# Performance work log

Hardware: AMD Instinct MI355X
Metric: run time of the kernel (lower is better)

Reference implementation:

```python
import jax, jax.numpy as jnp
import numpy as np
import math

N_EMBD = 1024
N_HEAD_DIM = 64
B, S = 8, 2048

def setup_inputs() -> dict:
    key = jax.random.key(0)
    ks = jax.random.split(key, 8)
    x = jax.random.normal(ks[0], (B, S, N_EMBD), dtype=jnp.float32)
    padding_mask = jax.random.randint(ks[1], (B, S), 0, 2).astype(jnp.bool_)
    scale = 1.0 / math.sqrt(N_EMBD)
    Wq = jax.random.normal(ks[2], (N_HEAD_DIM, N_EMBD), dtype=jnp.float32) * scale
    bq = jnp.zeros((N_HEAD_DIM,), dtype=jnp.float32)
    Wk = jax.random.normal(ks[3], (N_HEAD_DIM, N_EMBD), dtype=jnp.float32) * scale
    bk = jnp.zeros((N_HEAD_DIM,), dtype=jnp.float32)
    Wv = jax.random.normal(ks[4], (N_HEAD_DIM, N_EMBD), dtype=jnp.float32) * scale
    bv = jnp.zeros((N_HEAD_DIM,), dtype=jnp.float32)
    return {"x": x, "Wq": Wq, "bq": bq, "Wk": Wk, "bk": bk, "Wv": Wv, "bv": bv,
            "padding_mask": padding_mask}

def reference(x, Wq, bq, Wk, bk, Wv, bv, padding_mask):
    # q,k,v: [B,S,D] via Linear (x @ W^T + b)
    q = jnp.einsum('bse,de->bsd', x, Wq) + bq
    k = jnp.einsum('bse,de->bsd', x, Wk) + bk
    v = jnp.einsum('bse,de->bsd', x, Wv) + bv
    scale = 1.0 / math.sqrt(k.shape[-1])
    att = jnp.einsum('bqd,bkd->bqk', q, k) * scale  # [B,S,S]
    # padding_mask [B,S] -> [B,1,S]: True positions masked to -inf
    att = jnp.where(padding_mask[:, None, :], -jnp.inf, att)
    att = jax.nn.softmax(att, axis=-1)
    # attn_dropout omitted (eval mode / identity)
    return jnp.einsum('bqk,bkd->bqd', att, v)
```

## Files before the change

kernel.cpp:

```cpp
#include <hip/hip_runtime.h>
#include <hip/hip_bf16.h>

#define B_ 8
#define S_ 2048
#define E_ 1024
#define D_ 64
#define VT_STRIDE 2112

typedef short short8 __attribute__((ext_vector_type(8)));
typedef short short4v __attribute__((ext_vector_type(4)));
typedef float floatx4 __attribute__((ext_vector_type(4)));

static __device__ __forceinline__ short bf16_bits(float f) {
    __hip_bfloat16 h = __float2bfloat16(f);
    return *reinterpret_cast<short*>(&h);
}
static __device__ __forceinline__ float bits_to_f(short s) {
    __hip_bfloat16 h = *reinterpret_cast<__hip_bfloat16*>(&s);
    return __bfloat162float(h);
}
static __device__ __forceinline__ void split8(const float* __restrict__ p,
                                              short8& hi, short8& lo) {
    #pragma unroll
    for (int j = 0; j < 8; j++) {
        float f = p[j];
        short h = bf16_bits(f);
        hi[j] = h;
        lo[j] = bf16_bits(f - bits_to_f(h));
    }
}
static __device__ __forceinline__ void split8v(const float v[8],
                                               short8& hi, short8& lo) {
    #pragma unroll
    for (int j = 0; j < 8; j++) {
        float f = v[j];
        short h = bf16_bits(f);
        hi[j] = h;
        lo[j] = bf16_bits(f - bits_to_f(h));
    }
}
static __device__ __forceinline__ void dma16(const void* src, void* lds_dst) {
    __builtin_amdgcn_global_load_lds(
        (const __attribute__((address_space(1))) unsigned int*)src,
        (__attribute__((address_space(3))) unsigned int*)lds_dst, 16, 0, 0);
}

__global__ __launch_bounds__(256) void prep_kernel(
    const float* __restrict__ Wq, const float* __restrict__ Wk,
    const float* __restrict__ Wv, short8* __restrict__ Wpk8,
    const void* __restrict__ mask_raw, float* __restrict__ maskf)
{
    __shared__ unsigned int red[256];
    if (blockIdx.x < 96) {
        const int t = blockIdx.x * 256 + threadIdx.x;
        const int l16  = t & 15;
        const int quad = (t >> 4) & 3;
        const int nb   = (t >> 6) & 3;
        const int m    = (t >> 8) % 3;
        const int e0c  = (t >> 8) / 3;
        const float* W = (m == 0) ? Wq : ((m == 1) ? Wk : Wv);
        short8 hi, lo;
        split8(W + (size_t)(nb * 16 + l16) * E_ + e0c * 32 + quad * 8, hi, lo);
        const size_t pos = (size_t)((e0c * 3 + m) * 2) * 256 + nb * 64 + quad * 16 + l16;
        Wpk8[pos]       = hi;
        Wpk8[pos + 256] = lo;
    } else {
        const unsigned int* w = (const unsigned int*)mask_raw;
        unsigned int local = 0;
        for (int i = threadIdx.x; i < 4096; i += 256) local |= w[i];
        red[threadIdx.x] = local;
        __syncthreads();
        for (int s = 128; s > 0; s >>= 1) {
            if (threadIdx.x < s) red[threadIdx.x] |= red[threadIdx.x + s];
            __syncthreads();
        }
        const unsigned int ov = red[0];
        const bool is_u8 = (ov > 1u) && ((ov >> 24) <= 1u);
        const int i = (blockIdx.x - 96) * 256 + threadIdx.x;
        int v;
        if (ov == 0u)      v = 0;
        else if (is_u8)    v = (int)((const unsigned char*)mask_raw)[i];
        else               v = (((const unsigned int*)mask_raw)[i] != 0u);
        maskf[i] = v ? -1e30f : 0.0f;
    }
}

__global__ __launch_bounds__(512, 4) void qkv_kernel(
    const float* __restrict__ x, const short8* __restrict__ Wpk8,
    const float* __restrict__ bq, const float* __restrict__ bk,
    const float* __restrict__ bv,
    short* __restrict__ Qhi, short* __restrict__ Qlo,
    short* __restrict__ Khi, short* __restrict__ Vt)
{
    __shared__ alignas(16) float  xs[2][1024];
    __shared__ alignas(16) short8 wt[2][1536];
    const int tid  = threadIdx.x;
    const int wave = tid >> 6;
    const int nb   = wave & 3;
    const int rt   = wave >> 2;
    const int lane = tid & 63;
    const int l16  = lane & 15;
    const int quad = lane >> 4;
    const int row0 = blockIdx.x * 32;

    const float* xsrc = x + (size_t)(row0 + (tid >> 3)) * E_ +
                        (((tid & 7) ^ ((tid >> 3) & 7)) * 4);

    floatx4 acc[3];
    #pragma unroll
    for (int m = 0; m < 3; m++) acc[m] = (floatx4){0.f,0.f,0.f,0.f};

    if (tid < 256) dma16(xsrc, &xs[0][tid * 4]);
    #pragma unroll
    for (int i = 0; i < 3; i++)
        dma16(Wpk8 + (size_t)i * 512 + tid, &wt[0][i * 512 + tid]);

    int buf = 0;
    for (int e0c = 0; e0c < 32; ++e0c) {
        __syncthreads();
        if (e0c + 1 < 32) {
            if (tid < 256) dma16(xsrc + (e0c + 1) * 32, &xs[buf ^ 1][tid * 4]);
            #pragma unroll
            for (int i = 0; i < 3; i++)
                dma16(Wpk8 + (size_t)(e0c + 1) * 1536 + i * 512 + tid,
                      &wt[buf ^ 1][i * 512 + tid]);
        }

        const int rr = rt * 16 + l16;
        const int rx = rr & 7;
        const float* xr = &xs[buf][rr * 32];
        float4 a0 = *reinterpret_cast<const float4*>(xr + (((2 * quad)     ^ rx) * 4));
        float4 a1 = *reinterpret_cast<const float4*>(xr + (((2 * quad + 1) ^ rx) * 4));
        float av[8] = {a0.x, a0.y, a0.z, a0.w, a1.x, a1.y, a1.z, a1.w};
        short8 ah, al;
        split8v(av, ah, al);

        #pragma unroll
        for (int m = 0; m < 3; m++) {
            short8 wh = wt[buf][(m * 2 + 0) * 256 + nb * 64 + lane];
            short8 wl = wt[buf][(m * 2 + 1) * 256 + nb * 64 + lane];
            acc[m] = __builtin_amdgcn_mfma_f32_16x16x32_bf16(al, wh, acc[m], 0, 0, 0);
            acc[m] = __builtin_amdgcn_mfma_f32_16x16x32_bf16(ah, wl, acc[m], 0, 0, 0);
            acc[m] = __builtin_amdgcn_mfma_f32_16x16x32_bf16(ah, wh, acc[m], 0, 0, 0);
        }
        buf ^= 1;
    }

    const int d = nb * 16 + l16;
    const float bqv = bq[d];
    const float bkv = bk[d];
    const float bvv = bv[d];
    const int bch = row0 >> 11;
    const int rowbase = row0 + rt * 16 + quad * 4;
    short4v vpk;
    #pragma unroll
    for (int r = 0; r < 4; r++) {
        const size_t row = (size_t)(rowbase + r);
        const float q = (acc[0][r] + bqv) * 0.125f;
        const short qhv = bf16_bits(q);
        Qhi[row * 64 + d] = qhv;
        Qlo[row * 64 + d] = bf16_bits(q - bits_to_f(qhv));
        Khi[row * 64 + d] = bf16_bits(acc[1][r] + bkv);
        vpk[r] = bf16_bits(acc[2][r] + bvv);
    }
    *reinterpret_cast<short4v*>(Vt + ((size_t)(bch * 64 + d)) * VT_STRIDE +
                                (rowbase & 2047)) = vpk;
}

__global__ __launch_bounds__(256, 1) void attn_kernel(
    const short* __restrict__ Qhi, const short* __restrict__ Qlo,
    const short* __restrict__ Khi, const short* __restrict__ Vt,
    const float* __restrict__ maskf, float* __restrict__ out)
{
    __shared__ alignas(16) short8 kts[2][512];
    __shared__ alignas(16) short8 vts[2][512];
    __shared__ short PlT[4][16][72];

    const int tid  = threadIdx.x;
    const int wave = tid >> 6;
    const int lane = tid & 63;
    const int l16  = lane & 15;
    const int quad = lane >> 4;
    const int b    = blockIdx.x >> 5;
    const int qt   = blockIdx.x & 31;
    const size_t qbase  = (size_t)b * S_ + qt * 64 + wave * 16;
    const size_t kplane = (size_t)b * S_;
    const short* Vb = Vt + (size_t)b * 64 * VT_STRIDE;

    short8 qh[2], ql[2];
    #pragma unroll
    for (int dc = 0; dc < 2; dc++) {
        qh[dc] = *reinterpret_cast<const short8*>(Qhi + (qbase + l16) * 64 + dc * 32 + quad * 8);
        ql[dc] = *reinterpret_cast<const short8*>(Qlo + (qbase + l16) * 64 + dc * 32 + quad * 8);
    }

    float m = -1e30f, l = 0.f;
    floatx4 O[4];
    #pragma unroll
    for (int ob = 0; ob < 4; ob++) O[ob] = (floatx4){0.f,0.f,0.f,0.f};

    #pragma unroll
    for (int i = 0; i < 2; i++) {
        const int c = i * 256 + tid;
        const int r = c >> 3, cs = c & 7;
        dma16(Khi + (kplane + r) * 64 + ((cs ^ (r & 7)) * 8), &kts[0][c]);
        dma16(Vb + (size_t)r * VT_STRIDE + ((cs ^ (r & 7)) * 8), &vts[0][c]);
    }
    float4 mk4[4];
    #pragma unroll
    for (int kb = 0; kb < 4; kb++)
        mk4[kb] = *reinterpret_cast<const float4*>(maskf + kplane + kb * 16 + quad * 4);

    int buf = 0;
    for (int t = 0; t < 32; ++t) {
        __syncthreads();
        if (t + 1 < 32) {
            const int ktn = (t + 1) * 64;
            #pragma unroll
            for (int i = 0; i < 2; i++) {
                const int c = i * 256 + tid;
                const int r = c >> 3, cs = c & 7;
                dma16(Khi + (kplane + ktn + r) * 64 + ((cs ^ (r & 7)) * 8), &kts[buf ^ 1][c]);
                dma16(Vb + (size_t)r * VT_STRIDE + ktn + ((cs ^ (r & 7)) * 8), &vts[buf ^ 1][c]);
            }
        }

        floatx4 sc[4];
        #pragma unroll
        for (int kb = 0; kb < 4; kb++) {
            floatx4 a = (floatx4){0.f,0.f,0.f,0.f};
            #pragma unroll
            for (int kc = 0; kc < 2; kc++) {
                const int key = kb * 16 + l16;
                short8 kf = kts[buf][key * 8 + ((kc * 4 + quad) ^ (key & 7))];
                a = __builtin_amdgcn_mfma_f32_16x16x32_bf16(kf, qh[kc], a, 0, 0, 0);
                a = __builtin_amdgcn_mfma_f32_16x16x32_bf16(kf, ql[kc], a, 0, 0, 0);
            }
            sc[kb] = a;
        }
        #pragma unroll
        for (int kb = 0; kb < 4; kb++) {
            const float* mkp = reinterpret_cast<const float*>(&mk4[kb]);
            #pragma unroll
            for (int r = 0; r < 4; r++) sc[kb][r] += mkp[r];
        }

        float mx = -1e30f;
        #pragma unroll
        for (int kb = 0; kb < 4; kb++)
            #pragma unroll
            for (int r = 0; r < 4; r++) mx = fmaxf(mx, sc[kb][r]);
        mx = fmaxf(mx, __shfl_xor(mx, 16, 64));
        mx = fmaxf(mx, __shfl_xor(mx, 32, 64));
        const float mnew  = fmaxf(fmaxf(m, mx), -1e29f);
        const float alpha = __expf(m - mnew);
        float ps = 0.f;
        #pragma unroll
        for (int kb = 0; kb < 4; kb++)
            #pragma unroll
            for (int r = 0; r < 4; r++) {
                const float pe = __expf(sc[kb][r] - mnew);
                sc[kb][r] = pe;
                ps += pe;
            }
        ps += __shfl_xor(ps, 16, 64);
        ps += __shfl_xor(ps, 32, 64);
        l = l * alpha + ps;
        m = mnew;
        #pragma unroll
        for (int ob = 0; ob < 4; ob++) O[ob] *= alpha;

        #pragma unroll
        for (int kb = 0; kb < 4; kb++)
            #pragma unroll
            for (int r = 0; r < 4; r++)
                PlT[wave][l16][kb * 16 + quad * 4 + r] = bf16_bits(sc[kb][r]);
        short8 pf[2];
        #pragma unroll
        for (int kc = 0; kc < 2; kc++)
            pf[kc] = *reinterpret_cast<const short8*>(&PlT[wave][l16][kc * 32 + quad * 8]);

        #pragma unroll
        for (int ob = 0; ob < 4; ob++)
            #pragma unroll
            for (int kc = 0; kc < 2; kc++) {
                const int dd = ob * 16 + l16;
                short8 vf = vts[buf][dd * 8 + ((kc * 4 + quad) ^ (dd & 7))];
                O[ob] = __builtin_amdgcn_mfma_f32_16x16x32_bf16(vf, pf[kc], O[ob], 0, 0, 0);
            }

        if (t + 1 < 32) {
            const int ktn = (t + 1) * 64;
            #pragma unroll
            for (int kb = 0; kb < 4; kb++)
                mk4[kb] = *reinterpret_cast<const float4*>(
                    maskf + kplane + ktn + kb * 16 + quad * 4);
        }
        buf ^= 1;
    }

    #pragma unroll
    for (int ob = 0; ob < 4; ob++)
        #pragma unroll
        for (int r = 0; r < 4; r++)
            out[(qbase + l16) * 64 + ob * 16 + quad * 4 + r] = O[ob][r] / l;
}

extern "C" void kernel_launch(void* const* d_in, const int* in_sizes, int n_in,
                              void* d_out, int out_size, void* d_ws, size_t ws_size,
                              hipStream_t stream) {
    const float* x  = (const float*)d_in[0];
    const float* Wq = (const float*)d_in[1];
    const float* bq = (const float*)d_in[2];
    const float* Wk = (const float*)d_in[3];
    const float* bk = (const float*)d_in[4];
    const float* Wv = (const float*)d_in[5];
    const float* bv = (const float*)d_in[6];
    const void* mask = d_in[7];

    char* ws = (char*)d_ws;
    const size_t PLANE = (size_t)B_ * S_ * D_;
    short* Wpk = (short*)ws;
    short* Qhi = (short*)(ws + 768 * 1024);
    short* Qlo = Qhi + PLANE;
    short* Khi = Qlo + PLANE;
    short* Vt  = Khi + PLANE;
    float* maskf = (float*)(Vt + (size_t)512 * VT_STRIDE);

    prep_kernel<<<160, 256, 0, stream>>>(Wq, Wk, Wv, (short8*)Wpk, mask, maskf);
    qkv_kernel<<<512, 512, 0, stream>>>(x, (const short8*)Wpk, bq, bk, bv,
                                        Qhi, Qlo, Khi, Vt);
    attn_kernel<<<256, 256, 0, stream>>>(Qhi, Qlo, Khi, Vt, maskf,
                                         (float*)d_out);
}
```

Baseline: 187.9 us.

## Split attention keys across wave pairs and merge partial softmax in LDS

Each block now handles 32 queries instead of 64. Its four waves form two pairs, and each pair processes alternating 64-key tiles of a 128-key stage. Partial outputs, running max and running sum go to shared memory and are combined with a log-sum-exp rescale at the end. The grid doubles to 512 blocks and launch bounds allow 2 blocks per CU, giving more parallelism on a GPU that previously had only 256 blocks. In exchange, each block loads K/V tiles for fewer queries, which doubles total K/V traffic, and the merge adds an extra LDS step and synchronisation.

```diff
diff --git a/kernel.cpp b/kernel.cpp
--- a/kernel.cpp
+++ b/kernel.cpp
@@ -167,23 +167,32 @@
                                 (rowbase & 2047)) = vpk;
 }
 
-__global__ __launch_bounds__(256, 1) void attn_kernel(
+union alignas(16) AttnLds {
+    struct { short8 kts[4][512]; short8 vts[4][512]; } st;
+    struct {
+        float Osh[4][16][65];
+        float msh[4][16], lsh[4][16];
+    } mg;
+};
+
+__global__ __launch_bounds__(256, 2) void attn_kernel(
     const short* __restrict__ Qhi, const short* __restrict__ Qlo,
     const short* __restrict__ Khi, const short* __restrict__ Vt,
     const float* __restrict__ maskf, float* __restrict__ out)
 {
-    __shared__ alignas(16) short8 kts[2][512];
-    __shared__ alignas(16) short8 vts[2][512];
+    __shared__ AttnLds lds;
     __shared__ short PlT[4][16][72];
 
     const int tid  = threadIdx.x;
     const int wave = tid >> 6;
+    const int qsub = wave & 1;
+    const int par  = wave >> 1;
     const int lane = tid & 63;
     const int l16  = lane & 15;
     const int quad = lane >> 4;
-    const int b    = blockIdx.x >> 5;
-    const int qt   = blockIdx.x & 31;
-    const size_t qbase  = (size_t)b * S_ + qt * 64 + wave * 16;
+    const int b    = blockIdx.x >> 6;
+    const int qt   = blockIdx.x & 63;
+    const size_t qbase  = (size_t)b * S_ + qt * 32 + qsub * 16;
     const size_t kplane = (size_t)b * S_;
     const short* Vb = Vt + (size_t)b * 64 * VT_STRIDE;
 
@@ -200,30 +209,43 @@
     for (int ob = 0; ob < 4; ob++) O[ob] = (floatx4){0.f,0.f,0.f,0.f};
 
     #pragma unroll
-    for (int i = 0; i < 2; i++) {
-        const int c = i * 256 + tid;
-        const int r = c >> 3, cs = c & 7;
-        dma16(Khi + (kplane + r) * 64 + ((cs ^ (r & 7)) * 8), &kts[0][c]);
-        dma16(Vb + (size_t)r * VT_STRIDE + ((cs ^ (r & 7)) * 8), &vts[0][c]);
+    for (int p = 0; p < 2; p++) {
+        #pragma unroll
+        for (int i = 0; i < 2; i++) {
+            const int c = i * 256 + tid;
+            const int r = c >> 3, cs = c & 7;
+            dma16(Khi + (kplane + p * 64 + r) * 64 + ((cs ^ (r & 7)) * 8),
+                  &lds.st.kts[p][c]);
+            dma16(Vb + (size_t)r * VT_STRIDE + p * 64 + ((cs ^ (r & 7)) * 8),
+                  &lds.st.vts[p][c]);
+        }
     }
     float4 mk4[4];
     #pragma unroll
     for (int kb = 0; kb < 4; kb++)
-        mk4[kb] = *reinterpret_cast<const float4*>(maskf + kplane + kb * 16 + quad * 4);
-
-    int buf = 0;
-    for (int t = 0; t < 32; ++t) {
+        mk4[kb] = *reinterpret_cast<const float4*>(
+            maskf + kplane + par * 64 + kb * 16 + quad * 4);
+
+    for (int R = 0; R < 16; ++R) {
         __syncthreads();
-        if (t + 1 < 32) {
-            const int ktn = (t + 1) * 64;
-            #pragma unroll
-            for (int i = 0; i < 2; i++) {
-                const int c = i * 256 + tid;
-                const int r = c >> 3, cs = c & 7;
-                dma16(Khi + (kplane + ktn + r) * 64 + ((cs ^ (r & 7)) * 8), &kts[buf ^ 1][c]);
-                dma16(Vb + (size_t)r * VT_STRIDE + ktn + ((cs ^ (r & 7)) * 8), &vts[buf ^ 1][c]);
+        const int set = R & 1;
+        if (R + 1 < 16) {
+            const int nset = set ^ 1;
+            const int kt2 = (R + 1) * 128;
+            #pragma unroll
+            for (int p = 0; p < 2; p++) {
+                #pragma unroll
+                for (int i = 0; i < 2; i++) {
+                    const int c = i * 256 + tid;
+                    const int r = c >> 3, cs = c & 7;
+                    dma16(Khi + (kplane + kt2 + p * 64 + r) * 64 + ((cs ^ (r & 7)) * 8),
+                          &lds.st.kts[nset * 2 + p][c]);
+                    dma16(Vb + (size_t)r * VT_STRIDE + kt2 + p * 64 + ((cs ^ (r & 7)) * 8),
+                          &lds.st.vts[nset * 2 + p][c]);
+                }
             }
         }
+        const int buf = set * 2 + par;
 
         floatx4 sc[4];
         #pragma unroll
@@ -232,7 +254,7 @@
             #pragma unroll
             for (int kc = 0; kc < 2; kc++) {
                 const int key = kb * 16 + l16;
-                short8 kf = kts[buf][key * 8 + ((kc * 4 + quad) ^ (key & 7))];
+                short8 kf = lds.st.kts[buf][key * 8 + ((kc * 4 + quad) ^ (key & 7))];
                 a = __builtin_amdgcn_mfma_f32_16x16x32_bf16(kf, qh[kc], a, 0, 0, 0);
                 a = __builtin_amdgcn_mfma_f32_16x16x32_bf16(kf, ql[kc], a, 0, 0, 0);
             }
@@ -243,6 +265,14 @@
             const float* mkp = reinterpret_cast<const float*>(&mk4[kb]);
             #pragma unroll
             for (int r = 0; r < 4; r++) sc[kb][r] += mkp[r];
+        }
+
+        if (R + 1 < 16) {
+            const int ktn = (R + 1) * 128 + par * 64;
+            #pragma unroll
+            for (int kb = 0; kb < 4; kb++)
+                mk4[kb] = *reinterpret_cast<const float4*>(
+                    maskf + kplane + ktn + kb * 16 + quad * 4);
         }
 
         float mx = -1e30f;
@@ -285,25 +315,36 @@
             #pragma unroll
             for (int kc = 0; kc < 2; kc++) {
                 const int dd = ob * 16 + l16;
-                short8 vf = vts[buf][dd * 8 + ((kc * 4 + quad) ^ (dd & 7))];
+                short8 vf = lds.st.vts[buf][dd * 8 + ((kc * 4 + quad) ^ (dd & 7))];
                 O[ob] = __builtin_amdgcn_mfma_f32_16x16x32_bf16(vf, pf[kc], O[ob], 0, 0, 0);
             }
-
-        if (t + 1 < 32) {
-            const int ktn = (t + 1) * 64;
-            #pragma unroll
-            for (int kb = 0; kb < 4; kb++)
-                mk4[kb] = *reinterpret_cast<const float4*>(
-                    maskf + kplane + ktn + kb * 16 + quad * 4);
-        }
-        buf ^= 1;
-    }
-
+    }
+
+    __syncthreads();
     #pragma unroll
     for (int ob = 0; ob < 4; ob++)
         #pragma unroll
         for (int r = 0; r < 4; r++)
-            out[(qbase + l16) * 64 + ob * 16 + quad * 4 + r] = O[ob][r] / l;
+            lds.mg.Osh[wave][l16][ob * 16 + quad * 4 + r] = O[ob][r];
+    if (quad == 0) {
+        lds.mg.msh[wave][l16] = m;
+        lds.mg.lsh[wave][l16] = l;
+    }
+    __syncthreads();
+
+    #pragma unroll
+    for (int part = 0; part < 8; part++) {
+        const int idx = part * 256 + tid;
+        const int q = idx >> 6;
+        const int d = idx & 63;
+        const int w0 = (q >> 4), qq = q & 15;
+        const float m0 = lds.mg.msh[w0][qq], m1 = lds.mg.msh[w0 + 2][qq];
+        const float ms = fmaxf(m0, m1);
+        const float x0 = __expf(m0 - ms), x1 = __expf(m1 - ms);
+        const float lt = lds.mg.lsh[w0][qq] * x0 + lds.mg.lsh[w0 + 2][qq] * x1;
+        const float oa = lds.mg.Osh[w0][qq][d] * x0 + lds.mg.Osh[w0 + 2][qq][d] * x1;
+        out[((size_t)b * S_ + qt * 32 + q) * 64 + d] = oa / lt;
+    }
 }
 
 extern "C" void kernel_launch(void* const* d_in, const int* in_sizes, int n_in,
@@ -330,6 +371,6 @@
     prep_kernel<<<160, 256, 0, stream>>>(Wq, Wk, Wv, (short8*)Wpk, mask, maskf);
     qkv_kernel<<<512, 512, 0, stream>>>(x, (const short8*)Wpk, bq, bk, bv,
                                         Qhi, Qlo, Khi, Vt);
-    attn_kernel<<<256, 256, 0, stream>>>(Qhi, Qlo, Khi, Vt, maskf,
+    attn_kernel<<<512, 256, 0, stream>>>(Qhi, Qlo, Khi, Vt, maskf,
                                          (float*)d_out);
 }
```

Result: faster. 168.1 us (-10.5%).
